# Kernel optimization log

Hardware: AMD Instinct MI355X
Metric: run time of the kernel (lower is better)

Reference implementation:

```python
import jax, jax.numpy as jnp
import numpy as np

N, D, S, C = 2048, 1024, 49, 1000


def setup_inputs() -> dict:
    key = jax.random.key(0)
    k1, k2, k3 = jax.random.split(key, 3)
    x = jax.random.normal(k1, (N, D, S), dtype=jnp.float32)
    mu = jax.random.normal(k2, (C, D), dtype=jnp.float32)
    # precision = inverse covariance -> symmetric PSD; build a well-conditioned one
    R = jax.random.normal(k3, (D, D), dtype=jnp.float32)
    precision = (R @ R.T) / D + jnp.eye(D, dtype=jnp.float32)
    return {"x": x, "mu": mu, "precision": precision}


def reference(x, mu, precision):
    # z: [N, D] global-average-pooled features (z.view(N, D, -1).mean(2))
    z = jnp.mean(x, axis=2)
    # score[n, c] = -0.5 * (z_n - mu_c) @ P @ (z_n - mu_c)
    # Expanded to avoid materializing [N, C, D]:
    #   zPz - z P mu - mu P z + mu P mu   (no symmetry assumption on P)
    zP = z @ precision                      # [N, D]
    zPt = z @ precision.T                   # [N, D]
    qz = jnp.sum(zP * z, axis=1)            # [N]   diag(z P z^T)
    cross1 = zP @ mu.T                      # [N, C] z P mu
    cross2 = zPt @ mu.T                     # [N, C] mu P z
    qmu = jnp.einsum('cd,de,ce->c', mu, precision, mu)  # [C]
    score = -0.5 * (qz[:, None] - cross1 - cross2 + qmu[None, :])
    return score
```

## Files before the change

kernel.cpp:

```cpp
#include <hip/hip_runtime.h>
#include <hip/hip_bf16.h>

typedef unsigned short u16;
typedef __bf16 bf16x8 __attribute__((ext_vector_type(8)));
typedef float f32x4 __attribute__((ext_vector_type(4)));

typedef const __attribute__((address_space(1))) void gv_t;
typedef __attribute__((address_space(3))) void lv_t;

#define NN 2048
#define DD 1024
#define SS 49
#define CC 1000
#define CP 1024

#define POOL_BLOCKS ((NN * DD) / 256)
#define PREP_BLOCKS ((DD * DD) / 256)

__device__ inline u16 f2bf(float f) {
    __hip_bfloat16 h = __float2bfloat16(f);
    union { __hip_bfloat16 h; u16 u; } cv; cv.h = h; return cv.u;
}

__global__ __launch_bounds__(256) void pool_prep_k(const float* __restrict__ x,
                                                   const float* __restrict__ P,
                                                   const float* __restrict__ mu,
                                                   float* __restrict__ zf,
                                                   u16* __restrict__ zb,
                                                   u16* __restrict__ q,
                                                   u16* __restrict__ ab,
                                                   float* __restrict__ qzh,
                                                   float* __restrict__ qmuh) {
    __shared__ float lds[256 * SS];
    const int tid = threadIdx.x;
    if (blockIdx.x < POOL_BLOCKS) {
        const size_t base = (size_t)blockIdx.x * (256 * SS);
        const float4* src = (const float4*)(x + base);
        float4* dst = (float4*)lds;
        #pragma unroll
        for (int i = 0; i < 13; i++) {
            int idx = i * 256 + tid;
            if (idx < (256 * SS) / 4) dst[idx] = src[idx];
        }
        __syncthreads();
        const float* r = lds + tid * SS;
        float s = 0.f;
        #pragma unroll
        for (int j = 0; j < SS; j++) s += r[j];
        s *= (1.f / (float)SS);
        size_t o = (size_t)blockIdx.x * 256 + tid;
        zf[o] = s;
        zb[o] = f2bf(s);
    } else {
        int i = (blockIdx.x - POOL_BLOCKS) * 256 + tid;
        int r = i >> 10, c = i & 1023;
        q[i]  = f2bf(P[i] + P[c * DD + r]);
        ab[i] = f2bf(r < CC ? mu[i] : 0.f);
        if (i < NN) qzh[i]  = 0.f;
        if (i < CP) qmuh[i] = 0.f;
    }
}

#define BM 64
#define BN 64
#define BK 64

template <int MODE>
__global__ __launch_bounds__(256) void gemm_bt(const u16* __restrict__ A,
                                               const u16* __restrict__ Bt,
                                               int N, int K, int nbn,
                                               u16* __restrict__ Cb,
                                               const float* __restrict__ muf,
                                               const float* __restrict__ zf,
                                               float* __restrict__ qmuh_w,
                                               float* __restrict__ qzh_w,
                                               const float* __restrict__ qzr,
                                               const float* __restrict__ qmr,
                                               float* __restrict__ So, int cvalid) {
    __shared__ char As[2][BM * BK * 2];
    __shared__ char Bs[2][BN * BK * 2];
    const int tid = threadIdx.x;
    const int bm = blockIdx.x / nbn, bn = blockIdx.x % nbn;
    const int m0 = bm * BM, n0 = bn * BN;
    const int lane = tid & 63, w = tid >> 6;
    const int wr = w >> 1, wc = w & 1;
    const int r16 = lane & 15, hk = lane >> 4;

    f32x4 acc[2][2] = {};
    const char* Ab = (const char*)A;
    const char* Bb = (const char*)Bt;

    auto stage = [&](int buf, int k0) {
        #pragma unroll
        for (int j = 0; j < 2; j++) {
            const int c = j * 256 + tid;
            const int row = c >> 3, slot = c & 7;
            const int goff = ((slot ^ (row & 7)) << 4);
            __builtin_amdgcn_global_load_lds(
                (gv_t*)(Ab + ((size_t)(m0 + row) * K + k0) * 2 + goff),
                (lv_t*)(As[buf] + c * 16), 16, 0, 0);
            __builtin_amdgcn_global_load_lds(
                (gv_t*)(Bb + ((size_t)(n0 + row) * K + k0) * 2 + goff),
                (lv_t*)(Bs[buf] + c * 16), 16, 0, 0);
        }
    };

    const int nt = K / BK;
    stage(0, 0);
    __syncthreads();
    int cur = 0;
    for (int t = 0; t < nt; ++t) {
        if (t + 1 < nt) stage(cur ^ 1, (t + 1) * BK);
        bf16x8 a[2][2], b[2][2];
        #pragma unroll
        for (int mi = 0; mi < 2; mi++) {
            const int row = wr * 32 + mi * 16 + r16;
            #pragma unroll
            for (int kk = 0; kk < 2; kk++) {
                const int g = kk * 4 + hk;
                a[mi][kk] = *(const bf16x8*)(As[cur] + row * 128 + ((g ^ (row & 7)) << 4));
            }
        }
        #pragma unroll
        for (int ni = 0; ni < 2; ni++) {
            const int row = wc * 32 + ni * 16 + r16;
            #pragma unroll
            for (int kk = 0; kk < 2; kk++) {
                const int g = kk * 4 + hk;
                b[ni][kk] = *(const bf16x8*)(Bs[cur] + row * 128 + ((g ^ (row & 7)) << 4));
            }
        }
        #pragma unroll
        for (int kk = 0; kk < 2; kk++)
            #pragma unroll
            for (int mi = 0; mi < 2; mi++)
                #pragma unroll
                for (int ni = 0; ni < 2; ni++)
                    acc[mi][ni] = __builtin_amdgcn_mfma_f32_16x16x32_bf16(
                        a[mi][kk], b[ni][kk], acc[mi][ni], 0, 0, 0);
        __syncthreads();
        cur ^= 1;
    }

    const int cr = hk * 4, cc = r16;
    if (MODE == 2) {
        #pragma unroll
        for (int mi = 0; mi < 2; mi++) {
            #pragma unroll
            for (int ni = 0; ni < 2; ni++) {
                const int gr = m0 + wr * 32 + mi * 16 + cr;
                const int gc = n0 + wc * 32 + ni * 16 + cc;
                if (gc < cvalid) {
                    float qm = qmr[gc];
                    #pragma unroll
                    for (int r = 0; r < 4; r++)
                        So[(size_t)(gr + r) * cvalid + gc] =
                            0.5f * acc[mi][ni][r] - qzr[gr + r] - qm;
                }
            }
        }
    } else {
        const bool isMu = (m0 < CP);
        const float* S = isMu ? muf : zf;
        float* dst = isMu ? qmuh_w : qzh_w;
        #pragma unroll
        for (int mi = 0; mi < 2; mi++) {
            const int gr0 = m0 + wr * 32 + mi * 16 + cr;
            const int rbase = isMu ? gr0 : gr0 - CP;
            #pragma unroll
            for (int r = 0; r < 4; r++) {
                const int row = rbase + r;
                float v = 0.f;
                #pragma unroll
                for (int ni = 0; ni < 2; ni++) {
                    const int gc = n0 + wc * 32 + ni * 16 + cc;
                    float av = acc[mi][ni][r];
                    v += av * S[(size_t)row * DD + gc];
                    if (isMu) Cb[(size_t)(gr0 + r) * N + gc] = f2bf(av);
                }
                #pragma unroll
                for (int m = 1; m < 16; m <<= 1) v += __shfl_xor(v, m);
                if (cc == 0) atomicAdd(dst + row, 0.25f * v);
            }
        }
    }
}

extern "C" void kernel_launch(void* const* d_in, const int* in_sizes, int n_in,
                              void* d_out, int out_size, void* d_ws, size_t ws_size,
                              hipStream_t stream) {
    const float* x  = (const float*)d_in[0];
    const float* mu = (const float*)d_in[1];
    const float* P  = (const float*)d_in[2];
    float* out = (float*)d_out;

    char* w = (char*)d_ws;
    u16*   ab    = (u16*)w;    w += (size_t)(CP + NN) * DD * 2;
    u16*   q_bf  = (u16*)w;    w += (size_t)DD * DD * 2;
    u16*   b_bf  = (u16*)w;    w += (size_t)CP * DD * 2;
    float* z_f32 = (float*)w;  w += (size_t)NN * DD * 4;
    float* qzh   = (float*)w;  w += (size_t)NN * 4;
    float* qmuh  = (float*)w;

    u16* z_bf = ab + (size_t)CP * DD;

    pool_prep_k<<<POOL_BLOCKS + PREP_BLOCKS, 256, 0, stream>>>(
        x, P, mu, z_f32, z_bf, q_bf, ab, qzh, qmuh);
    gemm_bt<3><<<((CP + NN) / BM) * (DD / BN), 256, 0, stream>>>(
        ab, q_bf, DD, DD, DD / BN, b_bf, mu, z_f32, qmuh, qzh,
        nullptr, nullptr, nullptr, 0);
    gemm_bt<2><<<(NN / BM) * (CP / BN), 256, 0, stream>>>(
        z_bf, b_bf, CP, DD, CP / BN, nullptr, nullptr, nullptr, nullptr, nullptr,
        qzh, qmuh, out, CC);
}
```

Baseline: 124.2 us.

## Overlap mu·Q GEMM with pooling and fuse score GEMM with z·Q quadratic

Restructures the pipeline into four kernels. The mu·Q GEMM now shares a launch with the x pooling, so the small GEMM hides behind the memory-bound pooling. The score GEMM (z·B) and the z·Q GEMM for qz now run in one launch because neither depends on the other. Since qz is only ready after that launch, scores are written to a padded partial buffer and a final elementwise kernel subtracts qz. This adds an extra pass over an N×1024 fp32 buffer and uses more LDS per block in the pool kernel (50 KB), which can lower occupancy.

```diff
diff --git a/kernel.cpp b/kernel.cpp
--- a/kernel.cpp
+++ b/kernel.cpp
@@ -14,79 +14,23 @@
 #define CC 1000
 #define CP 1024
 
-#define POOL_BLOCKS ((NN * DD) / 256)
-#define PREP_BLOCKS ((DD * DD) / 256)
+#define BK 64
+#define KK DD
 
 __device__ inline u16 f2bf(float f) {
     __hip_bfloat16 h = __float2bfloat16(f);
     union { __hip_bfloat16 h; u16 u; } cv; cv.h = h; return cv.u;
 }
 
-__global__ __launch_bounds__(256) void pool_prep_k(const float* __restrict__ x,
-                                                   const float* __restrict__ P,
-                                                   const float* __restrict__ mu,
-                                                   float* __restrict__ zf,
-                                                   u16* __restrict__ zb,
-                                                   u16* __restrict__ q,
-                                                   u16* __restrict__ ab,
-                                                   float* __restrict__ qzh,
-                                                   float* __restrict__ qmuh) {
-    __shared__ float lds[256 * SS];
-    const int tid = threadIdx.x;
-    if (blockIdx.x < POOL_BLOCKS) {
-        const size_t base = (size_t)blockIdx.x * (256 * SS);
-        const float4* src = (const float4*)(x + base);
-        float4* dst = (float4*)lds;
-        #pragma unroll
-        for (int i = 0; i < 13; i++) {
-            int idx = i * 256 + tid;
-            if (idx < (256 * SS) / 4) dst[idx] = src[idx];
-        }
-        __syncthreads();
-        const float* r = lds + tid * SS;
-        float s = 0.f;
-        #pragma unroll
-        for (int j = 0; j < SS; j++) s += r[j];
-        s *= (1.f / (float)SS);
-        size_t o = (size_t)blockIdx.x * 256 + tid;
-        zf[o] = s;
-        zb[o] = f2bf(s);
-    } else {
-        int i = (blockIdx.x - POOL_BLOCKS) * 256 + tid;
-        int r = i >> 10, c = i & 1023;
-        q[i]  = f2bf(P[i] + P[c * DD + r]);
-        ab[i] = f2bf(r < CC ? mu[i] : 0.f);
-        if (i < NN) qzh[i]  = 0.f;
-        if (i < CP) qmuh[i] = 0.f;
-    }
-}
-
-#define BM 64
-#define BN 64
-#define BK 64
-
-template <int MODE>
-__global__ __launch_bounds__(256) void gemm_bt(const u16* __restrict__ A,
-                                               const u16* __restrict__ Bt,
-                                               int N, int K, int nbn,
-                                               u16* __restrict__ Cb,
-                                               const float* __restrict__ muf,
-                                               const float* __restrict__ zf,
-                                               float* __restrict__ qmuh_w,
-                                               float* __restrict__ qzh_w,
-                                               const float* __restrict__ qzr,
-                                               const float* __restrict__ qmr,
-                                               float* __restrict__ So, int cvalid) {
-    __shared__ char As[2][BM * BK * 2];
-    __shared__ char Bs[2][BN * BK * 2];
-    const int tid = threadIdx.x;
-    const int bm = blockIdx.x / nbn, bn = blockIdx.x % nbn;
-    const int m0 = bm * BM, n0 = bn * BN;
-    const int lane = tid & 63, w = tid >> 6;
-    const int wr = w >> 1, wc = w & 1;
+__device__ __forceinline__ void gemm64_core(const u16* __restrict__ A,
+                                            const u16* __restrict__ Bt,
+                                            int m0, int n0, char* smem,
+                                            f32x4 acc[2][2], int tid) {
+    char* As = smem;
+    char* Bs = smem + 16384;
+    const int lane = tid & 63;
+    const int wr = (tid >> 6) >> 1, wc = (tid >> 6) & 1;
     const int r16 = lane & 15, hk = lane >> 4;
-
-    f32x4 acc[2][2] = {};
     const char* Ab = (const char*)A;
     const char* Bb = (const char*)Bt;
 
@@ -97,93 +41,193 @@
             const int row = c >> 3, slot = c & 7;
             const int goff = ((slot ^ (row & 7)) << 4);
             __builtin_amdgcn_global_load_lds(
-                (gv_t*)(Ab + ((size_t)(m0 + row) * K + k0) * 2 + goff),
-                (lv_t*)(As[buf] + c * 16), 16, 0, 0);
+                (gv_t*)(Ab + ((size_t)(m0 + row) * KK + k0) * 2 + goff),
+                (lv_t*)(As + buf * 8192 + c * 16), 16, 0, 0);
             __builtin_amdgcn_global_load_lds(
-                (gv_t*)(Bb + ((size_t)(n0 + row) * K + k0) * 2 + goff),
-                (lv_t*)(Bs[buf] + c * 16), 16, 0, 0);
+                (gv_t*)(Bb + ((size_t)(n0 + row) * KK + k0) * 2 + goff),
+                (lv_t*)(Bs + buf * 8192 + c * 16), 16, 0, 0);
         }
     };
 
-    const int nt = K / BK;
+    const int nt = KK / BK;
     stage(0, 0);
     __syncthreads();
     int cur = 0;
-    for (int t = 0; t < nt; ++t) {
-        if (t + 1 < nt) stage(cur ^ 1, (t + 1) * BK);
+    for (int kt = 0; kt < nt; ++kt) {
+        if (kt + 1 < nt) stage(cur ^ 1, (kt + 1) * BK);
         bf16x8 a[2][2], b[2][2];
         #pragma unroll
         for (int mi = 0; mi < 2; mi++) {
             const int row = wr * 32 + mi * 16 + r16;
             #pragma unroll
-            for (int kk = 0; kk < 2; kk++) {
-                const int g = kk * 4 + hk;
-                a[mi][kk] = *(const bf16x8*)(As[cur] + row * 128 + ((g ^ (row & 7)) << 4));
+            for (int kk2 = 0; kk2 < 2; kk2++) {
+                const int g = kk2 * 4 + hk;
+                a[mi][kk2] = *(const bf16x8*)(As + cur * 8192 + row * 128 + ((g ^ (row & 7)) << 4));
             }
         }
         #pragma unroll
         for (int ni = 0; ni < 2; ni++) {
             const int row = wc * 32 + ni * 16 + r16;
             #pragma unroll
-            for (int kk = 0; kk < 2; kk++) {
-                const int g = kk * 4 + hk;
-                b[ni][kk] = *(const bf16x8*)(Bs[cur] + row * 128 + ((g ^ (row & 7)) << 4));
-            }
-        }
-        #pragma unroll
-        for (int kk = 0; kk < 2; kk++)
+            for (int kk2 = 0; kk2 < 2; kk2++) {
+                const int g = kk2 * 4 + hk;
+                b[ni][kk2] = *(const bf16x8*)(Bs + cur * 8192 + row * 128 + ((g ^ (row & 7)) << 4));
+            }
+        }
+        #pragma unroll
+        for (int kk2 = 0; kk2 < 2; kk2++)
             #pragma unroll
             for (int mi = 0; mi < 2; mi++)
                 #pragma unroll
                 for (int ni = 0; ni < 2; ni++)
                     acc[mi][ni] = __builtin_amdgcn_mfma_f32_16x16x32_bf16(
-                        a[mi][kk], b[ni][kk], acc[mi][ni], 0, 0, 0);
+                        a[mi][kk2], b[ni][kk2], acc[mi][ni], 0, 0, 0);
         __syncthreads();
         cur ^= 1;
     }
-
-    const int cr = hk * 4, cc = r16;
-    if (MODE == 2) {
+}
+
+__global__ __launch_bounds__(256) void prep_k(const float* __restrict__ P,
+                                              const float* __restrict__ mu,
+                                              u16* __restrict__ q,
+                                              u16* __restrict__ mu_bf,
+                                              float* __restrict__ qzh,
+                                              float* __restrict__ qmuh) {
+    int i = blockIdx.x * 256 + threadIdx.x;
+    int r = i >> 10, c = i & 1023;
+    q[i]     = f2bf(P[i] + P[c * DD + r]);
+    mu_bf[i] = f2bf(r < CC ? mu[i] : 0.f);
+    if (i < NN) qzh[i]  = 0.f;
+    if (i < CP) qmuh[i] = 0.f;
+}
+
+__global__ __launch_bounds__(256) void pool_muq_k(const float* __restrict__ x,
+                                                  const u16* __restrict__ q,
+                                                  const u16* __restrict__ mu_bf,
+                                                  const float* __restrict__ mu,
+                                                  u16* __restrict__ b_bf,
+                                                  float* __restrict__ qmuh,
+                                                  float* __restrict__ zf,
+                                                  u16* __restrict__ zb) {
+    __shared__ char smem[50176];
+    const int tid = threadIdx.x;
+    const int bid = blockIdx.x;
+
+    if (bid >= 256) {
+        const int u = bid - 256;
+        float* lds = (float*)smem;
+        const size_t base = (size_t)u * (256 * SS);
+        const float4* src = (const float4*)(x + base);
+        float4* dst = (float4*)lds;
+        #pragma unroll
+        for (int i = 0; i < 13; i++) {
+            int idx = i * 256 + tid;
+            if (idx < (256 * SS) / 4) dst[idx] = src[idx];
+        }
+        __syncthreads();
+        const float* r = lds + tid * SS;
+        float s = 0.f;
+        #pragma unroll
+        for (int j = 0; j < SS; j++) s += r[j];
+        s *= (1.f / 49.f);
+        size_t o = (size_t)u * 256 + tid;
+        zf[o] = s;
+        zb[o] = f2bf(s);
+        return;
+    }
+
+    const int m0 = (bid >> 4) * 64, n0 = (bid & 15) * 64;
+    f32x4 acc[2][2] = {};
+    gemm64_core(mu_bf, q, m0, n0, smem, acc, tid);
+
+    const int lane = tid & 63;
+    const int wr = (tid >> 6) >> 1, wc = (tid >> 6) & 1;
+    const int cr = (lane >> 4) * 4, cc2 = lane & 15;
+    #pragma unroll
+    for (int mi = 0; mi < 2; mi++) {
+        const int gr0 = m0 + wr * 32 + mi * 16 + cr;
+        #pragma unroll
+        for (int r = 0; r < 4; r++) {
+            const int row = gr0 + r;
+            float v = 0.f;
+            #pragma unroll
+            for (int ni = 0; ni < 2; ni++) {
+                const int gc = n0 + wc * 32 + ni * 16 + cc2;
+                float av = acc[mi][ni][r];
+                float sv = (row < CC) ? mu[(size_t)row * DD + gc] : 0.f;
+                v += av * sv;
+                b_bf[(size_t)row * DD + gc] = f2bf(av);
+            }
+            #pragma unroll
+            for (int m = 1; m < 16; m <<= 1) v += __shfl_xor(v, m);
+            if (cc2 == 0) atomicAdd(qmuh + row, 0.25f * v);
+        }
+    }
+}
+
+__global__ __launch_bounds__(256) void zgemm_k(const u16* __restrict__ z_bf,
+                                               const u16* __restrict__ q,
+                                               const u16* __restrict__ b_bf,
+                                               const float* __restrict__ zf,
+                                               const float* __restrict__ qmuh,
+                                               float* __restrict__ qzh,
+                                               float* __restrict__ part) {
+    __shared__ char smem[32768];
+    const int tid = threadIdx.x;
+    const int bid = blockIdx.x;
+    const bool isScore = (bid < 512);
+    const int i = isScore ? bid : bid - 512;
+    const int m0 = (i >> 4) * 64, n0 = (i & 15) * 64;
+
+    f32x4 acc[2][2] = {};
+    gemm64_core(z_bf, isScore ? b_bf : q, m0, n0, smem, acc, tid);
+
+    const int lane = tid & 63;
+    const int wr = (tid >> 6) >> 1, wc = (tid >> 6) & 1;
+    const int cr = (lane >> 4) * 4, cc2 = lane & 15;
+    if (isScore) {
         #pragma unroll
         for (int mi = 0; mi < 2; mi++) {
             #pragma unroll
             for (int ni = 0; ni < 2; ni++) {
                 const int gr = m0 + wr * 32 + mi * 16 + cr;
-                const int gc = n0 + wc * 32 + ni * 16 + cc;
-                if (gc < cvalid) {
-                    float qm = qmr[gc];
-                    #pragma unroll
-                    for (int r = 0; r < 4; r++)
-                        So[(size_t)(gr + r) * cvalid + gc] =
-                            0.5f * acc[mi][ni][r] - qzr[gr + r] - qm;
-                }
+                const int gc = n0 + wc * 32 + ni * 16 + cc2;
+                const float qm = qmuh[gc];
+                #pragma unroll
+                for (int r = 0; r < 4; r++)
+                    part[(size_t)(gr + r) * CP + gc] = 0.5f * acc[mi][ni][r] - qm;
             }
         }
     } else {
-        const bool isMu = (m0 < CP);
-        const float* S = isMu ? muf : zf;
-        float* dst = isMu ? qmuh_w : qzh_w;
         #pragma unroll
         for (int mi = 0; mi < 2; mi++) {
             const int gr0 = m0 + wr * 32 + mi * 16 + cr;
-            const int rbase = isMu ? gr0 : gr0 - CP;
             #pragma unroll
             for (int r = 0; r < 4; r++) {
-                const int row = rbase + r;
+                const int row = gr0 + r;
                 float v = 0.f;
                 #pragma unroll
                 for (int ni = 0; ni < 2; ni++) {
-                    const int gc = n0 + wc * 32 + ni * 16 + cc;
-                    float av = acc[mi][ni][r];
-                    v += av * S[(size_t)row * DD + gc];
-                    if (isMu) Cb[(size_t)(gr0 + r) * N + gc] = f2bf(av);
+                    const int gc = n0 + wc * 32 + ni * 16 + cc2;
+                    v += acc[mi][ni][r] * zf[(size_t)row * DD + gc];
                 }
                 #pragma unroll
                 for (int m = 1; m < 16; m <<= 1) v += __shfl_xor(v, m);
-                if (cc == 0) atomicAdd(dst + row, 0.25f * v);
-            }
-        }
-    }
+                if (cc2 == 0) atomicAdd(qzh + row, 0.25f * v);
+            }
+        }
+    }
+}
+
+__global__ __launch_bounds__(256) void finish_k(const float* __restrict__ part,
+                                                const float* __restrict__ qzh,
+                                                float* __restrict__ out) {
+    const int n = blockIdx.x, tid = threadIdx.x;
+    if (tid >= 250) return;
+    const float qz = qzh[n];
+    float4 p = *(const float4*)(part + (size_t)n * CP + tid * 4);
+    float4 o = { p.x - qz, p.y - qz, p.z - qz, p.w - qz };
+    *(float4*)(out + (size_t)n * CC + tid * 4) = o;
 }
 
 extern "C" void kernel_launch(void* const* d_in, const int* in_sizes, int n_in,
@@ -195,21 +239,18 @@
     float* out = (float*)d_out;
 
     char* w = (char*)d_ws;
-    u16*   ab    = (u16*)w;    w += (size_t)(CP + NN) * DD * 2;
-    u16*   q_bf  = (u16*)w;    w += (size_t)DD * DD * 2;
-    u16*   b_bf  = (u16*)w;    w += (size_t)CP * DD * 2;
-    float* z_f32 = (float*)w;  w += (size_t)NN * DD * 4;
-    float* qzh   = (float*)w;  w += (size_t)NN * 4;
+    u16*   q_bf  = (u16*)w;   w += (size_t)DD * DD * 2;
+    u16*   mu_bf = (u16*)w;   w += (size_t)CP * DD * 2;
+    u16*   b_bf  = (u16*)w;   w += (size_t)CP * DD * 2;
+    u16*   z_bf  = (u16*)w;   w += (size_t)NN * DD * 2;
+    float* zf    = (float*)w; w += (size_t)NN * DD * 4;
+    float* part  = (float*)w; w += (size_t)NN * CP * 4;
+    float* qzh   = (float*)w; w += (size_t)NN * 4;
     float* qmuh  = (float*)w;
 
-    u16* z_bf = ab + (size_t)CP * DD;
-
-    pool_prep_k<<<POOL_BLOCKS + PREP_BLOCKS, 256, 0, stream>>>(
-        x, P, mu, z_f32, z_bf, q_bf, ab, qzh, qmuh);
-    gemm_bt<3><<<((CP + NN) / BM) * (DD / BN), 256, 0, stream>>>(
-        ab, q_bf, DD, DD, DD / BN, b_bf, mu, z_f32, qmuh, qzh,
-        nullptr, nullptr, nullptr, 0);
-    gemm_bt<2><<<(NN / BM) * (CP / BN), 256, 0, stream>>>(
-        z_bf, b_bf, CP, DD, CP / BN, nullptr, nullptr, nullptr, nullptr, nullptr,
-        qzh, qmuh, out, CC);
-}
+    prep_k<<<(DD * DD) / 256, 256, 0, stream>>>(P, mu, q_bf, mu_bf, qzh, qmuh);
+    pool_muq_k<<<256 + (NN * DD) / 256, 256, 0, stream>>>(
+        x, q_bf, mu_bf, mu, b_bf, qmuh, zf, z_bf);
+    zgemm_k<<<1024, 256, 0, stream>>>(z_bf, q_bf, b_bf, zf, qmuh, qzh, part);
+    finish_k<<<NN, 256, 0, stream>>>(part, qzh, out);
+}
```

Measured after the change: 119.3 us. 4.0% less time.
